# Kernel optimization log

Hardware: AMD Instinct MI355X
Metric: run time of the kernel (lower is better)

## Reference

```python
import jax, jax.numpy as jnp
import numpy as np


def _patches3x3(x):
    # x: [B,H,W,C] -> [B,H,W,9,C], SAME zero padding, patch index k = i*3+j
    B, H, W, C = x.shape
    p = jnp.pad(x, ((0, 0), (1, 1), (1, 1), (0, 0)))
    return jnp.stack([p[:, i:i + H, j:j + W, :] for i in range(3) for j in range(3)], axis=3)


def setup_inputs() -> dict:
    key = jax.random.key(0)
    k1, k2, k3 = jax.random.split(key, 3)
    B, H, W, CH, NC, DIM = 4, 80, 80, 256, 22, 256
    x = jax.random.normal(k1, (B, H, W, CH), dtype=jnp.float32)
    seg_mask = jax.random.uniform(k2, (B, H, W, NC), dtype=jnp.float32)
    # he_uniform over receptive field ch*3*3
    lim = np.sqrt(6.0 / (CH * 9)).astype(np.float32)
    conv_w = jax.random.uniform(k3, (CH, 3, 3, DIM), dtype=jnp.float32, minval=-lim, maxval=lim)
    return {"x": x, "seg_mask": seg_mask, "conv_w": conv_w}


def reference(x, seg_mask, conv_w):
    B, H, W, CH = x.shape
    NC = seg_mask.shape[-1]
    DIM = conv_w.shape[-1]
    # patches of segmentation map: [B,H,W,9,NC]
    s_patch = _patches3x3(seg_mask)
    m = seg_mask[:, :, :, None, :]                       # [B,H,W,1,NC]
    s_max = jnp.max(m, axis=-1, keepdims=True)           # [B,H,W,1,1]
    # keep patch values only for the argmax class at the center pixel
    sel = jnp.sum(jnp.where(m == s_max, s_patch, 0.0), axis=-1)  # [B,H,W,9]
    cnt = jnp.sum((sel != 0.0).astype(jnp.float32), axis=-1, keepdims=True)  # [B,H,W,1]
    norm = jnp.where(cnt > 0, 9.0 / jnp.maximum(cnt, 1.0), 0.0)  # divide_no_nan(9, cnt)
    # per-channel 3x3 patch extraction of features (== depthwise conv with eye(9))
    xp = _patches3x3(x)                                  # [B,H,W,9,CH]
    xp = xp * sel[..., None]                             # mask-gated patches
    w = conv_w.reshape(CH, 9, DIM)
    out = jnp.einsum('bhwkc,ckd->bhwd', xp, w) * norm    # [B,H,W,DIM]
    return out
```

## Files before the change

### kernel.cpp

```cpp
#include <hip/hip_runtime.h>
#include <hip/hip_bf16.h>
#include <cstdint>

#define B_ 4
#define H_ 80
#define W_ 80
#define CH_ 256
#define NC_ 22
#define DIM_ 256
#define NPIX (B_*H_*W_)

typedef unsigned short ushort;
typedef __attribute__((ext_vector_type(8))) short short8;
typedef __attribute__((ext_vector_type(4))) float floatx4;

__device__ __attribute__((aligned(256))) static const unsigned char zglob[256] = {};

static __device__ inline ushort f2bf(float v) {
    __hip_bfloat16 h = __float2bfloat16(v);
    ushort r;
    __builtin_memcpy(&r, &h, 2);
    return r;
}
static __device__ inline unsigned pk2(float a, float b) {
    return (unsigned)f2bf(a) | ((unsigned)f2bf(b) << 16);
}
static __device__ inline void gll16(const void* g, void* l) {
    __builtin_amdgcn_global_load_lds((const __attribute__((address_space(1))) void*)g,
                                     (__attribute__((address_space(3))) void*)l, 16, 0, 0);
}

__global__ __launch_bounds__(256) void prep(const float* __restrict__ seg,
                                            const float* __restrict__ cw,
                                            const float* __restrict__ x,
                                            float* __restrict__ ssel,
                                            ushort* __restrict__ wbT,
                                            ushort* __restrict__ xb)
{
    __shared__ ushort ls[32][260];
    if (blockIdx.x < 900) {
        const int t = blockIdx.x * 256 + threadIdx.x;
        const int k = t / NPIX;
        const int m = t - k * NPIX;
        const int w = m % W_;
        const int h = (m / W_) % H_;
        const int b = m / (W_ * H_);

        const float2* c2 = (const float2*)(seg + (size_t)m * NC_);
        float cv[NC_];
        #pragma unroll
        for (int c = 0; c < NC_ / 2; ++c) { float2 v = c2[c]; cv[2*c] = v.x; cv[2*c+1] = v.y; }
        float mx = -1e30f;
        #pragma unroll
        for (int c = 0; c < NC_; ++c) mx = fmaxf(mx, cv[c]);

        const int i = k / 3, j = k % 3;
        const int hh = h + i - 1, ww = w + j - 1;
        float s = 0.f;
        if (hh >= 0 && hh < H_ && ww >= 0 && ww < W_) {
            const float2* n2 = (const float2*)(seg + ((size_t)((b * H_ + hh) * W_ + ww)) * NC_);
            #pragma unroll
            for (int c = 0; c < NC_ / 2; ++c) {
                float2 v = n2[c];
                s += (cv[2*c]   == mx) ? v.x : 0.f;
                s += (cv[2*c+1] == mx) ? v.y : 0.f;
            }
        }
        ssel[t] = s;
    } else if (blockIdx.x < 972) {
        const int bx = blockIdx.x - 900;
        const int k  = bx / 8;
        const int c0 = (bx % 8) * 32;
        const int c    = threadIdx.x >> 3;
        const int seg8 = threadIdx.x & 7;

        const float* src = cw + ((size_t)(c0 + c) * 9 + k) * DIM_ + seg8 * 32;
        #pragma unroll
        for (int e = 0; e < 32; e += 4) {
            float4 v = *(const float4*)(src + e);
            unsigned* dst = (unsigned*)&ls[c][seg8 * 32 + e];
            dst[0] = pk2(v.x, v.y);
            dst[1] = pk2(v.z, v.w);
        }
        __syncthreads();

        const int d = threadIdx.x;
        ushort tmp[32];
        #pragma unroll
        for (int cc = 0; cc < 32; ++cc) tmp[cc] = ls[cc][d];
        uint4 o[4];
        __builtin_memcpy(o, tmp, 64);
        uint4* dst = (uint4*)(wbT + ((size_t)k * 256 + d) * 256 + c0);
        dst[0] = o[0]; dst[1] = o[1]; dst[2] = o[2]; dst[3] = o[3];
    } else if (xb != nullptr) {
        size_t idx = ((size_t)(blockIdx.x - 972) * 256 + threadIdx.x) * 8;
        const float4* s = (const float4*)(x + idx);
        float4 a = s[0], b = s[1];
        uint4 o = make_uint4(pk2(a.x, a.y), pk2(a.z, a.w), pk2(b.x, b.y), pk2(b.z, b.w));
        *(uint4*)(xb + idx) = o;
    }
}

__global__ __launch_bounds__(256, 3) void conv2(const ushort* __restrict__ xb,
                                                const float* __restrict__ ssel,
                                                const ushort* __restrict__ wbT,
                                                float* __restrict__ out)
{
    __shared__ __attribute__((aligned(1024))) ushort xs[2][80 * 128];
    __shared__ float sl[9][80];

    const int tid  = threadIdx.x;
    const int lane = tid & 63;
    const int wv   = tid >> 6;
    const int ln   = lane & 15;
    const int quad = lane >> 4;
    const int rt   = blockIdx.x;
    const int b    = rt / H_;
    const int h    = rt % H_;
    const int d0   = blockIdx.y * 128;

    floatx4 O[5][2];
    #pragma unroll
    for (int i = 0; i < 5; ++i)
        #pragma unroll
        for (int jn = 0; jn < 2; ++jn)
            O[i][jn] = (floatx4){0.f, 0.f, 0.f, 0.f};

    short8 Breg[8];
    auto loadB = [&](int nit) {
        const int i   = nit / 6;
        const int rem = nit % 6;
        const int cc  = (rem / 3) * 128;
        const int jj  = rem % 3;
        const int k   = 3 * i + jj;
        #pragma unroll
        for (int kk = 0; kk < 4; ++kk)
            #pragma unroll
            for (int jn = 0; jn < 2; ++jn)
                Breg[kk * 2 + jn] = *(const short8*)(wbT
                    + ((size_t)k * 256 + d0 + wv * 32 + jn * 16 + ln) * 256
                    + cc + kk * 32 + quad * 8);
    };

    auto stage = [&](int nit) {
        const int i   = nit / 6;
        const int rem = nit % 6;
        const int cc  = (rem / 3) * 128;
        const int jj  = rem % 3;
        const int rr  = h + i - 1;
        const bool rowok = (rr >= 0) && (rr < H_);
        const ushort* xrow = xb + ((size_t)((b * H_ + (rowok ? rr : 0)) * W_)) * CH_ + cc;
        char* dbase = (char*)&xs[nit & 1][0];
        #pragma unroll
        for (int r = 0; r < 5; ++r) {
            const int s    = (r * 4 + wv) * 64 + lane;
            const int p    = s >> 4;
            const int cph  = s & 15;
            const int clog = cph ^ (p & 7);
            const int col  = p + jj - 1;
            const bool v   = rowok && (col >= 0) && (col < W_);
            const void* src = v ? (const void*)(xrow + (size_t)col * CH_ + clog * 8)
                                : (const void*)zglob;
            gll16(src, dbase + (size_t)(r * 4 + wv) * 1024);
        }
    };

    stage(0);
    loadB(0);
    if (tid < 80) {
        float rv[9]; int cnt = 0;
        #pragma unroll
        for (int k = 0; k < 9; ++k) {
            rv[k] = ssel[k * NPIX + rt * W_ + tid];
            cnt += (rv[k] != 0.f) ? 1 : 0;
        }
        const float norm = (cnt > 0) ? 9.f / (float)cnt : 0.f;
        #pragma unroll
        for (int k = 0; k < 9; ++k) sl[k][tid] = rv[k] * norm;
    }
    __syncthreads();

    #pragma unroll 2
    for (int it = 0; it < 18; ++it) {
        const int i   = it / 6;
        const int rem = it % 6;
        const int jj  = rem % 3;
        const int k   = 3 * i + jj;
        const char* bp = (const char*)&xs[it & 1][0];

        if (it < 17) stage(it + 1);

        floatx4 P[5][2];
        #pragma unroll
        for (int im = 0; im < 5; ++im)
            #pragma unroll
            for (int jn = 0; jn < 2; ++jn)
                P[im][jn] = (floatx4){0.f, 0.f, 0.f, 0.f};

        #pragma unroll
        for (int kk = 0; kk < 4; ++kk) {
            short8 a[5];
            #pragma unroll
            for (int im = 0; im < 5; ++im)
                a[im] = *(const short8*)(bp
                    + (size_t)(im * 16 + ln) * 256
                    + ((((kk << 2) | quad) ^ (ln & 7)) << 4));
            #pragma unroll
            for (int im = 0; im < 5; ++im)
                #pragma unroll
                for (int jn = 0; jn < 2; ++jn)
                    P[im][jn] = __builtin_amdgcn_mfma_f32_16x16x32_bf16(
                        a[im], Breg[kk * 2 + jn], P[im][jn], 0, 0, 0);
        }

        if (it < 17) loadB(it + 1);

        #pragma unroll
        for (int im = 0; im < 5; ++im) {
            const float4 sv = *(const float4*)&sl[k][im * 16 + quad * 4];
            #pragma unroll
            for (int jn = 0; jn < 2; ++jn) {
                O[im][jn][0] += sv.x * P[im][jn][0];
                O[im][jn][1] += sv.y * P[im][jn][1];
                O[im][jn][2] += sv.z * P[im][jn][2];
                O[im][jn][3] += sv.w * P[im][jn][3];
            }
        }
        __syncthreads();
    }

    #pragma unroll
    for (int im = 0; im < 5; ++im) {
        #pragma unroll
        for (int jn = 0; jn < 2; ++jn) {
            const int dd = d0 + wv * 32 + jn * 16 + ln;
            #pragma unroll
            for (int r = 0; r < 4; ++r) {
                const int m = im * 16 + quad * 4 + r;
                out[((size_t)(rt * W_ + m)) * DIM_ + dd] = O[im][jn][r];
            }
        }
    }
}

__global__ __launch_bounds__(256, 3) void conv2_fb(const float* __restrict__ x,
                                                   const float* __restrict__ ssel,
                                                   const ushort* __restrict__ wbT,
                                                   float* __restrict__ out)
{
    __shared__ ushort xsA[2][80 * 136];
    __shared__ float  sl[9][80];

    const int tid  = threadIdx.x;
    const int lane = tid & 63;
    const int wv   = tid >> 6;
    const int ln   = lane & 15;
    const int quad = lane >> 4;
    const int rt   = blockIdx.x;
    const int b    = rt / H_;
    const int h    = rt % H_;
    const int d0   = blockIdx.y * 128;

    int qm[5], qc[5];
    #pragma unroll
    for (int r = 0; r < 5; ++r) { int q = tid + 256 * r; qm[r] = q >> 4; qc[r] = q & 15; }

    floatx4 O[5][2];
    #pragma unroll
    for (int i = 0; i < 5; ++i)
        #pragma unroll
        for (int jn = 0; jn < 2; ++jn)
            O[i][jn] = (floatx4){0.f, 0.f, 0.f, 0.f};

    float4 fa[5], fb[5];
    bool   ok[5];

    auto stage_load = [&](int nit) {
        const int i = nit / 6, rem = nit % 6, cc = (rem / 3) * 128, jj = rem % 3;
        const int rr = h + i - 1;
        const bool rowok = (rr >= 0) && (rr < H_);
        const int rsafe = rowok ? rr : h;
        #pragma unroll
        for (int r = 0; r < 5; ++r) {
            const int col = qm[r] + jj - 1;
            const bool v = rowok && (col >= 0) && (col < W_);
            ok[r] = v;
            const float* f = x + ((size_t)(b * H_ + rsafe) * W_ + (v ? col : 0)) * CH_ + cc + qc[r] * 8;
            fa[r] = *(const float4*)f;
            fb[r] = *(const float4*)(f + 4);
        }
    };
    auto stage_write = [&](int nit) {
        ushort* bp = xsA[nit & 1];
        #pragma unroll
        for (int r = 0; r < 5; ++r) {
            uint4 v = ok[r] ? make_uint4(pk2(fa[r].x, fa[r].y), pk2(fa[r].z, fa[r].w),
                                         pk2(fb[r].x, fb[r].y), pk2(fb[r].z, fb[r].w))
                            : make_uint4(0u, 0u, 0u, 0u);
            *(uint4*)&bp[qm[r] * 136 + qc[r] * 8] = v;
        }
    };

    short8 Breg[8];
    auto loadB = [&](int nit) {
        const int i = nit / 6, rem = nit % 6, cc = (rem / 3) * 128, jj = rem % 3;
        const int k = 3 * i + jj;
        #pragma unroll
        for (int kk = 0; kk < 4; ++kk)
            #pragma unroll
            for (int jn = 0; jn < 2; ++jn)
                Breg[kk * 2 + jn] = *(const short8*)(wbT
                    + ((size_t)k * 256 + d0 + wv * 32 + jn * 16 + ln) * 256
                    + cc + kk * 32 + quad * 8);
    };

    stage_load(0);
    if (tid < 80) {
        float rv[9]; int cnt = 0;
        #pragma unroll
        for (int k = 0; k < 9; ++k) { rv[k] = ssel[k * NPIX + rt * W_ + tid]; cnt += (rv[k] != 0.f) ? 1 : 0; }
        const float norm = (cnt > 0) ? 9.f / (float)cnt : 0.f;
        #pragma unroll
        for (int k = 0; k < 9; ++k) sl[k][tid] = rv[k] * norm;
    }
    stage_write(0);
    loadB(0);
    __syncthreads();

    #pragma unroll 2
    for (int it = 0; it < 18; ++it) {
        const int i = it / 6, rem = it % 6, jj = rem % 3;
        const int k = 3 * i + jj;
        const ushort* bp = xsA[it & 1];

        if (it < 17) stage_load(it + 1);

        floatx4 P[5][2];
        #pragma unroll
        for (int im = 0; im < 5; ++im)
            #pragma unroll
            for (int jn = 0; jn < 2; ++jn)
                P[im][jn] = (floatx4){0.f, 0.f, 0.f, 0.f};

        #pragma unroll
        for (int kk = 0; kk < 4; ++kk) {
            short8 a[5];
            #pragma unroll
            for (int im = 0; im < 5; ++im)
                a[im] = *(const short8*)&bp[(im * 16 + ln) * 136 + kk * 32 + quad * 8];
            #pragma unroll
            for (int im = 0; im < 5; ++im)
                #pragma unroll
                for (int jn = 0; jn < 2; ++jn)
                    P[im][jn] = __builtin_amdgcn_mfma_f32_16x16x32_bf16(
                        a[im], Breg[kk * 2 + jn], P[im][jn], 0, 0, 0);
        }

        if (it < 17) stage_write(it + 1);
        if (it < 17) loadB(it + 1);

        #pragma unroll
        for (int im = 0; im < 5; ++im) {
            const float4 sv = *(const float4*)&sl[k][im * 16 + quad * 4];
            #pragma unroll
            for (int jn = 0; jn < 2; ++jn) {
                O[im][jn][0] += sv.x * P[im][jn][0];
                O[im][jn][1] += sv.y * P[im][jn][1];
                O[im][jn][2] += sv.z * P[im][jn][2];
                O[im][jn][3] += sv.w * P[im][jn][3];
            }
        }
        __syncthreads();
    }

    #pragma unroll
    for (int im = 0; im < 5; ++im)
        #pragma unroll
        for (int jn = 0; jn < 2; ++jn) {
            const int dd = d0 + wv * 32 + jn * 16 + ln;
            #pragma unroll
            for (int r = 0; r < 4; ++r) {
                const int m = im * 16 + quad * 4 + r;
                out[((size_t)(rt * W_ + m)) * DIM_ + dd] = O[im][jn][r];
            }
        }
}

extern "C" void kernel_launch(void* const* d_in, const int* in_sizes, int n_in,
                              void* d_out, int out_size, void* d_ws, size_t ws_size,
                              hipStream_t stream)
{
    const float* x   = (const float*)d_in[0];
    const float* seg = (const float*)d_in[1];
    const float* cw  = (const float*)d_in[2];
    float* out = (float*)d_out;

    float*  ssel = (float*)d_ws;
    ushort* wbT  = (ushort*)((char*)d_ws + 921600);
    ushort* xb   = (ushort*)((char*)d_ws + 921600 + 1179648);
    const size_t need = 921600u + 1179648u + 13107200u;

    if (ws_size >= need) {
        prep<<<dim3(972 + 3200), dim3(256), 0, stream>>>(seg, cw, x, ssel, wbT, xb);
        conv2<<<dim3(B_ * H_, 2), dim3(256), 0, stream>>>(xb, ssel, wbT, out);
    } else {
        prep<<<dim3(972), dim3(256), 0, stream>>>(seg, cw, x, ssel, wbT, nullptr);
        conv2_fb<<<dim3(B_ * H_, 2), dim3(256), 0, stream>>>(x, ssel, wbT, out);
    }
}
```

Measured before the change: 149.4 us.

## Stage haloed input row once and reuse it across three column taps

Each LDS stage now holds 82 padded pixels (84 allocated) of one input row and channel half. The three horizontal taps read it at shifted offsets instead of staging a separately shifted copy per tap. Staging drops from 18 to 6 per block, cutting global-to-LDS traffic and barriers roughly threefold. In exchange LDS use grows slightly, and the per-tap swizzle index is computed from the shifted pixel row, which may change bank-conflict behaviour.

```diff
diff --git a/kernel.cpp b/kernel.cpp
--- a/kernel.cpp
+++ b/kernel.cpp
@@ -106,7 +106,7 @@
                                                 const ushort* __restrict__ wbT,
                                                 float* __restrict__ out)
 {
-    __shared__ __attribute__((aligned(1024))) ushort xs[2][80 * 128];
+    __shared__ __attribute__((aligned(1024))) ushort xs[2][84 * 128];
     __shared__ float sl[9][80];
 
     const int tid  = threadIdx.x;
@@ -127,12 +127,7 @@
             O[i][jn] = (floatx4){0.f, 0.f, 0.f, 0.f};
 
     short8 Breg[8];
-    auto loadB = [&](int nit) {
-        const int i   = nit / 6;
-        const int rem = nit % 6;
-        const int cc  = (rem / 3) * 128;
-        const int jj  = rem % 3;
-        const int k   = 3 * i + jj;
+    auto loadB = [&](int k, int cc) {
         #pragma unroll
         for (int kk = 0; kk < 4; ++kk)
             #pragma unroll
@@ -142,31 +137,39 @@
                     + cc + kk * 32 + quad * 8);
     };
 
-    auto stage = [&](int nit) {
-        const int i   = nit / 6;
-        const int rem = nit % 6;
-        const int cc  = (rem / 3) * 128;
-        const int jj  = rem % 3;
-        const int rr  = h + i - 1;
+    auto stage = [&](int g) {
+        const int gi = g >> 1;
+        const int cc = (g & 1) * 128;
+        const int rr = h + gi - 1;
         const bool rowok = (rr >= 0) && (rr < H_);
         const ushort* xrow = xb + ((size_t)((b * H_ + (rowok ? rr : 0)) * W_)) * CH_ + cc;
-        char* dbase = (char*)&xs[nit & 1][0];
+        char* dbase = (char*)&xs[g & 1][0];
         #pragma unroll
         for (int r = 0; r < 5; ++r) {
-            const int s    = (r * 4 + wv) * 64 + lane;
+            const int e    = r * 4 + wv;
+            const int s    = e * 64 + lane;
             const int p    = s >> 4;
             const int cph  = s & 15;
             const int clog = cph ^ (p & 7);
-            const int col  = p + jj - 1;
-            const bool v   = rowok && (col >= 0) && (col < W_);
-            const void* src = v ? (const void*)(xrow + (size_t)col * CH_ + clog * 8)
+            const bool v   = rowok && (p >= 1) && (p <= 80);
+            const void* src = v ? (const void*)(xrow + (size_t)(p - 1) * CH_ + clog * 8)
                                 : (const void*)zglob;
-            gll16(src, dbase + (size_t)(r * 4 + wv) * 1024);
+            gll16(src, dbase + (size_t)e * 1024);
+        }
+        if (wv == 0) {
+            const int s    = 20 * 64 + lane;
+            const int p    = s >> 4;
+            const int cph  = s & 15;
+            const int clog = cph ^ (p & 7);
+            const bool v   = rowok && (p <= 80);
+            const void* src = v ? (const void*)(xrow + (size_t)(p - 1) * CH_ + clog * 8)
+                                : (const void*)zglob;
+            gll16(src, dbase + (size_t)20 * 1024);
         }
     };
 
     stage(0);
-    loadB(0);
+    loadB(0, 0);
     if (tid < 80) {
         float rv[9]; int cnt = 0;
         #pragma unroll
@@ -181,49 +184,55 @@
     __syncthreads();
 
     #pragma unroll 2
-    for (int it = 0; it < 18; ++it) {
-        const int i   = it / 6;
-        const int rem = it % 6;
-        const int jj  = rem % 3;
-        const int k   = 3 * i + jj;
-        const char* bp = (const char*)&xs[it & 1][0];
-
-        if (it < 17) stage(it + 1);
-
-        floatx4 P[5][2];
-        #pragma unroll
-        for (int im = 0; im < 5; ++im)
-            #pragma unroll
-            for (int jn = 0; jn < 2; ++jn)
-                P[im][jn] = (floatx4){0.f, 0.f, 0.f, 0.f};
-
-        #pragma unroll
-        for (int kk = 0; kk < 4; ++kk) {
-            short8 a[5];
-            #pragma unroll
-            for (int im = 0; im < 5; ++im)
-                a[im] = *(const short8*)(bp
-                    + (size_t)(im * 16 + ln) * 256
-                    + ((((kk << 2) | quad) ^ (ln & 7)) << 4));
+    for (int g = 0; g < 6; ++g) {
+        const int gi = g >> 1;
+        const int cc = (g & 1) * 128;
+        const char* bp = (const char*)&xs[g & 1][0];
+
+        if (g < 5) stage(g + 1);
+
+        #pragma unroll
+        for (int j = 0; j < 3; ++j) {
+            const int k = 3 * gi + j;
+
+            floatx4 P[5][2];
             #pragma unroll
             for (int im = 0; im < 5; ++im)
                 #pragma unroll
                 for (int jn = 0; jn < 2; ++jn)
-                    P[im][jn] = __builtin_amdgcn_mfma_f32_16x16x32_bf16(
-                        a[im], Breg[kk * 2 + jn], P[im][jn], 0, 0, 0);
-        }
-
-        if (it < 17) loadB(it + 1);
-
-        #pragma unroll
-        for (int im = 0; im < 5; ++im) {
-            const float4 sv = *(const float4*)&sl[k][im * 16 + quad * 4];
-            #pragma unroll
-            for (int jn = 0; jn < 2; ++jn) {
-                O[im][jn][0] += sv.x * P[im][jn][0];
-                O[im][jn][1] += sv.y * P[im][jn][1];
-                O[im][jn][2] += sv.z * P[im][jn][2];
-                O[im][jn][3] += sv.w * P[im][jn][3];
+                    P[im][jn] = (floatx4){0.f, 0.f, 0.f, 0.f};
+
+            #pragma unroll
+            for (int kk = 0; kk < 4; ++kk) {
+                short8 a[5];
+                #pragma unroll
+                for (int im = 0; im < 5; ++im) {
+                    const int p = im * 16 + ln + j;
+                    a[im] = *(const short8*)(bp
+                        + (size_t)p * 256
+                        + ((((kk << 2) | quad) ^ (p & 7)) << 4));
+                }
+                #pragma unroll
+                for (int im = 0; im < 5; ++im)
+                    #pragma unroll
+                    for (int jn = 0; jn < 2; ++jn)
+                        P[im][jn] = __builtin_amdgcn_mfma_f32_16x16x32_bf16(
+                            a[im], Breg[kk * 2 + jn], P[im][jn], 0, 0, 0);
+            }
+
+            if (j < 2)      loadB(k + 1, cc);
+            else if (g < 5) loadB(3 * ((g + 1) >> 1), ((g + 1) & 1) * 128);
+
+            #pragma unroll
+            for (int im = 0; im < 5; ++im) {
+                const float4 sv = *(const float4*)&sl[k][im * 16 + quad * 4];
+                #pragma unroll
+                for (int jn = 0; jn < 2; ++jn) {
+                    O[im][jn][0] += sv.x * P[im][jn][0];
+                    O[im][jn][1] += sv.y * P[im][jn][1];
+                    O[im][jn][2] += sv.z * P[im][jn][2];
+                    O[im][jn][3] += sv.w * P[im][jn][3];
+                }
             }
         }
         __syncthreads();
@@ -297,7 +306,8 @@
             uint4 v = ok[r] ? make_uint4(pk2(fa[r].x, fa[r].y), pk2(fa[r].z, fa[r].w),
                                          pk2(fb[r].x, fb[r].y), pk2(fb[r].z, fb[r].w))
                             : make_uint4(0u, 0u, 0u, 0u);
-            *(uint4*)&bp[qm[r] * 136 + qc[r] * 8] = v;
+            *(uint4*)&xsA[nit & 1][qm[r] * 136 + qc[r] * 8] = v;
+            (void)bp;
         }
     };
 
```

Result: slower. 247.3 us (+65.6%).
